# Optimization experiments

Measured on AMD Instinct MI355X. Metric: run time of the kernel, lower is better.

## Reference

```python
import jax, jax.numpy as jnp
import numpy as np

B, DIM, H, W = 8, 64, 128, 128
HEADS = 8
HID = DIM * 2          # ffn_expansion_factor = 2
DCONV = DIM // 4       # partial-conv channels
EPS_LN = 1e-5
EPS_NRM = 1e-12

def _conv(x, w, groups=1):
    # stride-1 conv, SAME padding (matches padding=1 for k=3, padding=0 for k=1)
    return jax.lax.conv_general_dilated(
        x, w, (1, 1), 'SAME',
        dimension_numbers=('NCHW', 'OIHW', 'NCHW'),
        feature_group_count=groups)

def _ln_channel(x, w, b):
    # WithBias LayerNorm over channel dim (to_3d puts c last, normalize last dim)
    mu = x.mean(axis=1, keepdims=True)
    var = ((x - mu) ** 2).mean(axis=1, keepdims=True)
    return (x - mu) / jnp.sqrt(var + EPS_LN) * w[None, :, None, None] + b[None, :, None, None]

def setup_inputs() -> dict:
    key = jax.random.key(0)
    ks = jax.random.split(key, 8)
    s = 0.02
    return {
        'x': jax.random.normal(ks[0], (B, DIM, H, W), jnp.float32),
        'ln1_w': jnp.ones((DIM,), jnp.float32),
        'ln1_b': jnp.zeros((DIM,), jnp.float32),
        'qkv_w': jax.random.normal(ks[1], (3 * DIM, DIM, 1, 1), jnp.float32) * s,
        'qkv_dw_w': jax.random.normal(ks[2], (3 * DIM, 1, 3, 3), jnp.float32) * s,
        'temperature': jnp.ones((HEADS, 1, 1), jnp.float32),
        'attn_mix': jnp.ones((2,), jnp.float32),
        'proj_w': jax.random.normal(ks[3], (DIM, DIM, 1, 1), jnp.float32) * s,
        'ln2_w': jnp.ones((DIM,), jnp.float32),
        'ln2_b': jnp.zeros((DIM,), jnp.float32),
        'pconv_w': jax.random.normal(ks[4], (DCONV, DCONV, 3, 3), jnp.float32) * s,
        'pin_w': jax.random.normal(ks[5], (2 * HID, DIM, 1, 1), jnp.float32) * s,
        'dw_w': jax.random.normal(ks[6], (HID, 1, 3, 3), jnp.float32) * s,
        'pout_w': jax.random.normal(ks[7], (DIM, HID, 1, 1), jnp.float32) * s,
    }

def reference(x, ln1_w, ln1_b, qkv_w, qkv_dw_w, temperature, attn_mix,
              proj_w, ln2_w, ln2_b, pconv_w, pin_w, dw_w, pout_w):
    b, c, h, w = x.shape
    ch = c // HEADS
    # ---- TwinPeakAttention on norm1(x) ----
    y = _ln_channel(x, ln1_w, ln1_b)
    qkv = _conv(_conv(y, qkv_w), qkv_dw_w, groups=3 * c)
    q, k, v = jnp.split(qkv, 3, axis=1)
    rs = lambda t: t.reshape(b, HEADS, ch, h * w)          # b head c (h w)
    q, k, v = rs(q), rs(k), rs(v)
    q = q / jnp.maximum(jnp.linalg.norm(q, axis=-1, keepdims=True), EPS_NRM)
    k = k / jnp.maximum(jnp.linalg.norm(k, axis=-1, keepdims=True), EPS_NRM)
    scores = jnp.einsum('bhcn,bhdn->bhcd', q, k)           # [b, head, ch, ch]
    attn_sm = jax.nn.softmax(scores * temperature[None], axis=-1)
    attn_relu = jnp.maximum(scores, 0.0) ** 2
    wmix = jax.nn.softmax(attn_mix)
    attn = wmix[0] * attn_sm + wmix[1] * attn_relu
    out = jnp.einsum('bhcd,bhdn->bhcn', attn, v).reshape(b, c, h, w)
    x = x + _conv(out, proj_w)
    # ---- FDFN on norm2(x) ----
    y = _ln_channel(x, ln2_w, ln2_b)
    y = jnp.concatenate([_conv(y[:, :DCONV], pconv_w), y[:, DCONV:]], axis=1)
    y = _conv(y, pin_w)                                    # [b, 2*HID, h, w]
    a, g = jnp.split(y, 2, axis=1)
    a = _conv(a, dw_w, groups=HID)
    y = _conv(jax.nn.gelu(a, approximate=False) * g, pout_w)
    return x + y
```

## Files before the change

kernel.cpp:

```cpp
#include <hip/hip_runtime.h>
#include <math.h>

#define NPIX 16384
#define B_ 8

typedef __attribute__((ext_vector_type(4))) float f32x4;
typedef __attribute__((ext_vector_type(8))) short bf16x8;
typedef __attribute__((ext_vector_type(4))) unsigned int u32x4;

__device__ inline unsigned short f2bf(float f) {
  unsigned int u = __builtin_bit_cast(unsigned int, f);
  return (unsigned short)((u + 0x7fffu + ((u >> 16) & 1u)) >> 16);
}
__device__ inline float bf2f(unsigned short h) {
  unsigned int u = ((unsigned int)h) << 16;
  return __builtin_bit_cast(float, u);
}
__device__ inline unsigned int pack2(unsigned short a, unsigned short b) {
  return (unsigned int)a | ((unsigned int)b << 16);
}
__device__ inline f32x4 mfma16(bf16x8 a, bf16x8 b, f32x4 c) {
  return __builtin_amdgcn_mfma_f32_16x16x32_bf16(a, b, c, 0, 0, 0);
}
__device__ inline void unpack8(u32x4 u, float* f) {
#pragma unroll
  for (int i = 0; i < 4; ++i) {
    unsigned int w = u[i];
    f[2 * i]     = __builtin_bit_cast(float, w << 16);
    f[2 * i + 1] = __builtin_bit_cast(float, w & 0xffff0000u);
  }
}


__global__ __launch_bounds__(256) void k0_prep(
    const float* __restrict__ wq, const float* __restrict__ lw,
    const float* __restrict__ lb, const float* __restrict__ pin,
    const float* __restrict__ pout, unsigned short* __restrict__ wq2,
    float* __restrict__ s1, float* __restrict__ s2,
    unsigned short* __restrict__ pinb, unsigned short* __restrict__ pob) {
  int bid = blockIdx.x, t = threadIdx.x;
  if (bid == 0) {
    if (t < 192) {
      int co = t;
      float a = 0.f, bsum = 0.f;
      for (int ci = 0; ci < 64; ++ci) {
        float w = wq[co * 64 + ci];
        unsigned short hb = f2bf(w * lw[ci]);
        wq2[co * 64 + ci] = hb;
        a += bf2f(hb);
        bsum = fmaf(w, lb[ci], bsum);
      }
      s1[co] = a;
      s2[co] = bsum;
    }
  } else if (bid <= 64) {
    int i = (bid - 1) * 256 + t;
    pinb[i] = f2bf(pin[i]);
  } else {
    int i = (bid - 65) * 256 + t;
    pob[i] = f2bf(pout[i]);
  }
}

__global__ __launch_bounds__(256) void k1_qkv(
    const float* __restrict__ x, const unsigned short* __restrict__ wq2,
    const float* __restrict__ s1, const float* __restrict__ s2,
    unsigned short* __restrict__ qkv) {
  __shared__ __align__(16) unsigned char lx[64 * 128];
  __shared__ float sumL[4][64], sqL[4][64], muL[64], rsL[64];
  __shared__ __align__(16) unsigned short epi[4][16][72];
  int t = threadIdx.x, blk = blockIdx.x;
  int b = blk >> 8, hw0 = (blk & 255) * 64;
  const float* xb = x + (size_t)b * 64 * NPIX + hw0;
  int p = t & 63, g8 = t >> 6;
  float psum = 0.f, psq = 0.f;
#pragma unroll
  for (int r = 0; r < 2; ++r) {
    int ci0 = g8 * 8 + r * 32;
    float v[8];
#pragma unroll
    for (int j = 0; j < 8; ++j) {
      v[j] = xb[(size_t)(ci0 + j) * NPIX + p];
      psum += v[j];
      psq = fmaf(v[j], v[j], psq);
    }
    u32x4 pk;
#pragma unroll
    for (int j = 0; j < 4; ++j) pk[j] = pack2(f2bf(v[2 * j]), f2bf(v[2 * j + 1]));
    unsigned int addr = ((unsigned)(p * 128 + ci0 * 2)) ^ ((p & 7) << 4);
    *(u32x4*)&lx[addr] = pk;
  }
  sumL[g8][p] = psum;
  sqL[g8][p] = psq;
  __syncthreads();
  if (t < 64) {
    float s = sumL[0][t] + sumL[1][t] + sumL[2][t] + sumL[3][t];
    float q = sqL[0][t] + sqL[1][t] + sqL[2][t] + sqL[3][t];
    float mu = s * (1.f / 64.f);
    float var = q * (1.f / 64.f) - mu * mu;
    muL[t] = mu;
    rsL[t] = rsqrtf(fmaxf(var, 0.f) + 1e-5f);
  }
  __syncthreads();
  int lane = t & 63, wv = t >> 6, l16 = lane & 15, g = lane >> 4;
  int co0 = wv * 48;
  bf16x8 A[3][2];
#pragma unroll
  for (int ct = 0; ct < 3; ++ct) {
    int co = co0 + ct * 16 + l16;
#pragma unroll
    for (int kh = 0; kh < 2; ++kh)
      A[ct][kh] = *(const bf16x8*)(wq2 + (size_t)co * 64 + kh * 32 + g * 8);
  }
  f32x4 acc[3][4];
#pragma unroll
  for (int ct = 0; ct < 3; ++ct)
#pragma unroll
    for (int nt = 0; nt < 4; ++nt) acc[ct][nt] = (f32x4)0.f;
#pragma unroll
  for (int nt = 0; nt < 4; ++nt) {
    int pp = nt * 16 + l16;
#pragma unroll
    for (int kh = 0; kh < 2; ++kh) {
      unsigned int addr = ((unsigned)(pp * 128 + (kh * 32 + g * 8) * 2)) ^ ((pp & 7) << 4);
      bf16x8 Bf = *(const bf16x8*)&lx[addr];
#pragma unroll
      for (int ct = 0; ct < 3; ++ct) acc[ct][nt] = mfma16(A[ct][kh], Bf, acc[ct][nt]);
    }
  }
  int row1 = hw0 >> 7, wb1 = hw0 & 127;
  unsigned short* ob = qkv + ((size_t)(b * 128 + row1) * 192) * 128 + wb1;
#pragma unroll
  for (int ct = 0; ct < 3; ++ct) {
#pragma unroll
    for (int r = 0; r < 4; ++r) {
      int co = co0 + ct * 16 + g * 4 + r;
      float s1v = s1[co], s2v = s2[co];
#pragma unroll
      for (int nt = 0; nt < 4; ++nt) {
        int pl = nt * 16 + l16;
        float val = (acc[ct][nt][r] - muL[pl] * s1v) * rsL[pl] + s2v;
        epi[wv][g * 4 + r][pl] = f2bf(val);
      }
    }
#pragma unroll
    for (int i = 0; i < 2; ++i) {
      int chunk = i * 64 + lane, co_l = chunk >> 3, oct = chunk & 7;
      u32x4 v = *(const u32x4*)&epi[wv][co_l][oct * 8];
      *(u32x4*)(ob + (size_t)(co0 + ct * 16 + co_l) * 128 + oct * 8) = v;
    }
  }
}

__global__ __launch_bounds__(256) void k2_dw3x3(
    const unsigned short* __restrict__ in, const float* __restrict__ w9,
    unsigned short* __restrict__ out) {
  int blk0 = blockIdx.x;
  int blk = (blk0 & 7) * 1536 + (blk0 >> 3);
  int id = blk * 256 + threadIdx.x;
  int oct = id & 15;
  int cr = id >> 4;
  int ch = cr % 192;
  int br = cr / 192;
  int row = br & 127;
  int w0 = oct * 8;
  const float* wp = w9 + ch * 9;
  float wgt[9];
#pragma unroll
  for (int j = 0; j < 9; ++j) wgt[j] = wp[j];
  float rowv[3][10];
#pragma unroll
  for (int dy = 0; dy < 3; ++dy) {
#pragma unroll
    for (int i = 0; i < 10; ++i) rowv[dy][i] = 0.f;
    int hh = row + dy - 1;
    if ((unsigned)hh < 128u) {
      const unsigned short* rp = in + ((size_t)(br + dy - 1) * 192 + ch) * 128 + w0;
      u32x4 m = *(const u32x4*)rp;
      unpack8(m, &rowv[dy][1]);
      if (w0 > 0) rowv[dy][0] = bf2f(rp[-1]);
      if (w0 < 120) rowv[dy][9] = bf2f(rp[8]);
    }
  }
  u32x4 res;
#pragma unroll
  for (int i = 0; i < 8; i += 2) {
    float a0 = 0.f, a1 = 0.f;
#pragma unroll
    for (int dy = 0; dy < 3; ++dy)
#pragma unroll
      for (int dx = 0; dx < 3; ++dx) {
        a0 = fmaf(wgt[dy * 3 + dx], rowv[dy][i + dx], a0);
        a1 = fmaf(wgt[dy * 3 + dx], rowv[dy][i + 1 + dx], a1);
      }
    res[i >> 1] = pack2(f2bf(a0), f2bf(a1));
  }
  *(u32x4*)(out + ((size_t)br * 192 + ch) * 128 + w0) = res;
}

__global__ __launch_bounds__(256) void k3a_mfma(
    const unsigned short* __restrict__ qkvd, float* __restrict__ parts) {
  __shared__ float red[4][640];
  int blk = blockIdx.x;
  int b = blk >> 6, chunk = blk & 63;
  int t = threadIdx.x;
  int lane = t & 63, wv = t >> 6, l16 = lane & 15, g = lane >> 4;
  const unsigned short* bb = qkvd + (size_t)(b * 128) * 192 * 128;
  int n0 = chunk * 256 + wv * 64;
  f32x4 S[4], QQ[4], KK[4];
#pragma unroll
  for (int i = 0; i < 4; ++i) { S[i] = (f32x4)0.f; QQ[i] = (f32x4)0.f; KK[i] = (f32x4)0.f; }
#pragma unroll
  for (int ks = 0; ks < 2; ++ks) {
    int k0 = n0 + ks * 32 + g * 8;
    int r = k0 >> 7, w = k0 & 127;
    const unsigned short* rowb = bb + ((size_t)r * 192) * 128 + w;
    bf16x8 Q[4], K[4];
#pragma unroll
    for (int t4 = 0; t4 < 4; ++t4) {
      Q[t4] = *(const bf16x8*)(rowb + (size_t)(t4 * 16 + l16) * 128);
      K[t4] = *(const bf16x8*)(rowb + (size_t)(64 + t4 * 16 + l16) * 128);
    }
#pragma unroll
    for (int t4 = 0; t4 < 4; ++t4) {
      S[t4]  = mfma16(Q[t4], K[t4], S[t4]);
      QQ[t4] = mfma16(Q[t4], Q[t4], QQ[t4]);
      KK[t4] = mfma16(K[t4], K[t4], KK[t4]);
    }
  }
  int hi = l16 >> 3;
#pragma unroll
  for (int t4 = 0; t4 < 4; ++t4) {
#pragma unroll
    for (int r = 0; r < 4; ++r) {
      int m = g * 4 + r;
      if ((m >> 3) == hi) {
        int head = 2 * t4 + hi;
        red[wv][head * 80 + 16 + (m & 7) * 8 + (l16 & 7)] = S[t4][r];
      }
      if (m == l16) {
        int c = t4 * 16 + l16;
        red[wv][(c >> 3) * 80 + (c & 7)] = QQ[t4][r];
        red[wv][(c >> 3) * 80 + 8 + (c & 7)] = KK[t4][r];
      }
    }
  }
  __syncthreads();
  float* pb = parts + (size_t)blk * 640;
  for (int i = t; i < 640; i += 256)
    pb[i] = red[0][i] + red[1][i] + red[2][i] + red[3][i];
}

__global__ __launch_bounds__(256) void k3bc(
    const float* __restrict__ parts, const float* __restrict__ temp,
    const float* __restrict__ mix, const float* __restrict__ pw,
    unsigned short* __restrict__ M) {
  int b = blockIdx.x, t = threadIdx.x;
  __shared__ float s[8][80];
  __shared__ float att[8][64];
  for (int i = t; i < 640; i += 256) {
    const float* pbase = parts + (size_t)b * 64 * 640 + i;
    float v = 0.f;
    for (int c = 0; c < 64; ++c) v += pbase[c * 640];
    s[i / 80][i % 80] = v;
  }
  __syncthreads();
  float m0 = fmaxf(mix[0], mix[1]);
  float e0 = expf(mix[0] - m0), e1 = expf(mix[1] - m0);
  float w0 = e0 / (e0 + e1), w1 = e1 / (e0 + e1);
  for (int i = t; i < 512; i += 256) {
    int head = i >> 6, e = i & 63, c = e >> 3, d = e & 7;
    float tt = temp[head];
    float rq = 1.f / fmaxf(sqrtf(s[head][c]), 1e-12f);
    float sc[8];
    float mx = -1e30f;
#pragma unroll
    for (int d2 = 0; d2 < 8; ++d2) {
      float rk = 1.f / fmaxf(sqrtf(s[head][8 + d2]), 1e-12f);
      sc[d2] = s[head][16 + c * 8 + d2] * rq * rk;
      mx = fmaxf(mx, sc[d2] * tt);
    }
    float sum = 0.f;
#pragma unroll
    for (int d2 = 0; d2 < 8; ++d2) sum += expf(sc[d2] * tt - mx);
    float sm = expf(sc[d] * tt - mx) / sum;
    float r = fmaxf(sc[d], 0.f);
    r = r * r;
    att[head][e] = w0 * sm + w1 * r;
  }
  __syncthreads();
  for (int i = t; i < 4096; i += 256) {
    int co = i >> 6, ci = i & 63, head = ci >> 3, d = ci & 7;
    float a = 0.f;
#pragma unroll
    for (int cc = 0; cc < 8; ++cc)
      a = fmaf(pw[co * 64 + head * 8 + cc], att[head][cc * 8 + d], a);
    M[(size_t)b * 4096 + i] = f2bf(a);
  }
}

__global__ __launch_bounds__(256) void k4_av(
    const unsigned short* __restrict__ qkvd, const unsigned short* __restrict__ Mb,
    const float* __restrict__ x, const float* __restrict__ lw,
    const float* __restrict__ lb, unsigned short* __restrict__ x1,
    unsigned short* __restrict__ y2) {
  __shared__ __align__(16) unsigned char lv[64 * 128];
  __shared__ float sumL[4][64], sqL[4][64], muL[64], rsL[64];
  int t = threadIdx.x, blk = blockIdx.x;
  int b = blk >> 8, hw0 = (blk & 255) * 64;
  int row4 = hw0 >> 7, wb4 = hw0 & 127;
  const unsigned short* vb = qkvd + ((size_t)(b * 128 + row4) * 192 + 128) * 128 + wb4;
  int p = t & 63, g8 = t >> 6;
#pragma unroll
  for (int r = 0; r < 2; ++r) {
    int ci0 = g8 * 8 + r * 32;
    unsigned short hh[8];
#pragma unroll
    for (int j = 0; j < 8; ++j) hh[j] = vb[(size_t)(ci0 + j) * 128 + p];
    u32x4 pk;
#pragma unroll
    for (int j = 0; j < 4; ++j) pk[j] = pack2(hh[2 * j], hh[2 * j + 1]);
    unsigned int addr = ((unsigned)(p * 128 + ci0 * 2)) ^ ((p & 7) << 4);
    *(u32x4*)&lv[addr] = pk;
  }
  __syncthreads();
  int lane = t & 63, wv = t >> 6, l16 = lane & 15, g = lane >> 4;
  bf16x8 A[2];
#pragma unroll
  for (int kh = 0; kh < 2; ++kh)
    A[kh] = *(const bf16x8*)(Mb + (size_t)b * 4096 + (size_t)(wv * 16 + l16) * 64 + kh * 32 + g * 8);
  f32x4 acc[4];
#pragma unroll
  for (int nt = 0; nt < 4; ++nt) acc[nt] = (f32x4)0.f;
#pragma unroll
  for (int nt = 0; nt < 4; ++nt) {
    int pp = nt * 16 + l16;
#pragma unroll
    for (int kh = 0; kh < 2; ++kh) {
      unsigned int addr = ((unsigned)(pp * 128 + (kh * 32 + g * 8) * 2)) ^ ((pp & 7) << 4);
      bf16x8 Bf = *(const bf16x8*)&lv[addr];
      acc[nt] = mfma16(A[kh], Bf, acc[nt]);
    }
  }
  const float* xb = x + (size_t)b * 64 * NPIX + hw0;
  unsigned short* x1b = x1 + (size_t)b * 64 * NPIX + hw0;
  float vals[4][4];
#pragma unroll
  for (int nt = 0; nt < 4; ++nt) {
    float ps = 0.f, pq = 0.f;
#pragma unroll
    for (int r = 0; r < 4; ++r) {
      int co = wv * 16 + g * 4 + r;
      size_t idx = (size_t)co * NPIX + nt * 16 + l16;
      float a = acc[nt][r] + xb[idx];
      vals[nt][r] = a;
      x1b[idx] = f2bf(a);
      ps += a;
      pq = fmaf(a, a, pq);
    }
    ps += __shfl_xor(ps, 16); ps += __shfl_xor(ps, 32);
    pq += __shfl_xor(pq, 16); pq += __shfl_xor(pq, 32);
    if (g == 0) { sumL[wv][nt * 16 + l16] = ps; sqL[wv][nt * 16 + l16] = pq; }
  }
  __syncthreads();
  if (t < 64) {
    float s = sumL[0][t] + sumL[1][t] + sumL[2][t] + sumL[3][t];
    float q = sqL[0][t] + sqL[1][t] + sqL[2][t] + sqL[3][t];
    float mu = s * (1.f / 64.f);
    float var = q * (1.f / 64.f) - mu * mu;
    muL[t] = mu;
    rsL[t] = rsqrtf(fmaxf(var, 0.f) + 1e-5f);
  }
  __syncthreads();
  unsigned short* y2b = y2 + (size_t)b * 64 * NPIX + hw0;
#pragma unroll
  for (int nt = 0; nt < 4; ++nt)
#pragma unroll
    for (int r = 0; r < 4; ++r) {
      int co = wv * 16 + g * 4 + r;
      int pl = nt * 16 + l16;
      float yv = (vals[nt][r] - muL[pl]) * rsL[pl] * lw[co] + lb[co];
      y2b[(size_t)co * NPIX + pl] = f2bf(yv);
    }
}

__global__ __launch_bounds__(256) void k5_pconv(
    const unsigned short* __restrict__ y2, const float* __restrict__ pcw,
    unsigned short* __restrict__ pc) {
  __shared__ unsigned short ly[16 * 120];
  int t = threadIdx.x, blk = blockIdx.x;
  int b = blk >> 8, tile = blk & 255;
  int ty = tile >> 4, tx = tile & 15;
  int h0 = ty * 8, w0 = tx * 8;
  const unsigned short* yb = y2 + (size_t)b * 64 * NPIX;
  for (int i = t; i < 1600; i += 256) {
    int ci = i / 100, r = i - ci * 100;
    int hy = r / 10, hx = r - hy * 10;
    int gh = h0 - 1 + hy, gw = w0 - 1 + hx;
    unsigned short v = 0;
    if ((unsigned)gh < 128u && (unsigned)gw < 128u) v = yb[(size_t)ci * NPIX + gh * 128 + gw];
    ly[ci * 120 + hy * 12 + hx] = v;
  }
  __syncthreads();
  int lp = t & 63;
  int py = lp >> 3, px = lp & 7;
  int cq = __builtin_amdgcn_readfirstlane(t >> 6);
  int co0 = cq * 4;
  float a0 = 0.f, a1 = 0.f, a2 = 0.f, a3 = 0.f;
  for (int ci = 0; ci < 16; ++ci) {
    float nb[9];
#pragma unroll
    for (int ky = 0; ky < 3; ++ky)
#pragma unroll
      for (int kx = 0; kx < 3; ++kx)
        nb[ky * 3 + kx] = bf2f(ly[ci * 120 + (py + ky) * 12 + px + kx]);
    const float* wp = pcw + (co0 * 16 + ci) * 9;
#pragma unroll
    for (int k = 0; k < 9; ++k) {
      a0 = fmaf(wp[k],       nb[k], a0);
      a1 = fmaf(wp[144 + k], nb[k], a1);
      a2 = fmaf(wp[288 + k], nb[k], a2);
      a3 = fmaf(wp[432 + k], nb[k], a3);
    }
  }
  size_t obase = (size_t)b * 16 * NPIX + (h0 + py) * 128 + w0 + px;
  pc[obase + (size_t)(co0 + 0) * NPIX] = f2bf(a0);
  pc[obase + (size_t)(co0 + 1) * NPIX] = f2bf(a1);
  pc[obase + (size_t)(co0 + 2) * NPIX] = f2bf(a2);
  pc[obase + (size_t)(co0 + 3) * NPIX] = f2bf(a3);
}

__global__ __launch_bounds__(256) void k6_pin(
    const unsigned short* __restrict__ pc, const unsigned short* __restrict__ y2,
    const unsigned short* __restrict__ pinb, unsigned short* __restrict__ ag) {
  __shared__ __align__(16) unsigned char bt[64 * 128];
  __shared__ __align__(16) unsigned short epi[4][16][72];
  int t = threadIdx.x, blk = blockIdx.x;
  int b = blk >> 8, hw0 = (blk & 255) * 64;
  int px = t & 63, cb = t >> 6;
  {
    const unsigned short* base = (cb == 0) ? (pc + (size_t)b * 16 * NPIX)
                                           : (y2 + (size_t)b * 64 * NPIX);
#pragma unroll
    for (int j = 0; j < 16; j += 2) {
      int ch = cb * 16 + j;
      unsigned short v0 = base[(size_t)ch * NPIX + hw0 + px];
      unsigned short v1 = base[(size_t)(ch + 1) * NPIX + hw0 + px];
      unsigned int addr = ((unsigned)(px * 128 + ch * 2)) ^ ((px & 7) << 4);
      *(unsigned int*)&bt[addr] = pack2(v0, v1);
    }
  }
  __syncthreads();
  int lane = t & 63, wv = t >> 6, l16 = lane & 15, g = lane >> 4;
  bf16x8 A[4][2];
#pragma unroll
  for (int ct = 0; ct < 4; ++ct) {
    int co = wv * 64 + ct * 16 + l16;
#pragma unroll
    for (int kh = 0; kh < 2; ++kh)
      A[ct][kh] = *(const bf16x8*)(pinb + (size_t)co * 64 + kh * 32 + g * 8);
  }
  f32x4 acc[4][4];
#pragma unroll
  for (int ct = 0; ct < 4; ++ct)
#pragma unroll
    for (int nt = 0; nt < 4; ++nt) acc[ct][nt] = (f32x4)0.f;
#pragma unroll
  for (int nt = 0; nt < 4; ++nt) {
    int pp = nt * 16 + l16;
#pragma unroll
    for (int kh = 0; kh < 2; ++kh) {
      unsigned int addr = ((unsigned)(pp * 128 + (kh * 32 + g * 8) * 2)) ^ ((pp & 7) << 4);
      bf16x8 Bf = *(const bf16x8*)&bt[addr];
#pragma unroll
      for (int ct = 0; ct < 4; ++ct) acc[ct][nt] = mfma16(A[ct][kh], Bf, acc[ct][nt]);
    }
  }
  int row6 = hw0 >> 7, wb6 = hw0 & 127;
  unsigned short* ab = ag + ((size_t)(b * 128 + row6) * 256) * 128 + wb6;
#pragma unroll
  for (int ct = 0; ct < 4; ++ct) {
#pragma unroll
    for (int nt = 0; nt < 4; ++nt)
#pragma unroll
      for (int r = 0; r < 4; ++r)
        epi[wv][g * 4 + r][nt * 16 + l16] = f2bf(acc[ct][nt][r]);
#pragma unroll
    for (int i = 0; i < 2; ++i) {
      int chunk = i * 64 + lane, co_l = chunk >> 3, oct = chunk & 7;
      u32x4 v = *(const u32x4*)&epi[wv][co_l][oct * 8];
      int co = wv * 64 + ct * 16 + co_l;
      *(u32x4*)(ab + (size_t)co * 128 + oct * 8) = v;
    }
  }
}

__global__ __launch_bounds__(256) void k7_fdfn(
    const unsigned short* __restrict__ ag, const float* __restrict__ dww,
    const unsigned short* __restrict__ pob, const unsigned short* __restrict__ x1,
    float* __restrict__ out) {
  __shared__ __align__(16) unsigned char bt[64 * 256];
  __shared__ float dwl[1152];
  int t = threadIdx.x;
  int blk0 = blockIdx.x;
  int blk = (blk0 & 7) * 256 + (blk0 >> 3);
  int b = blk >> 8, rr = blk & 255;
  int row = rr >> 1, w0t = (rr & 1) * 64;
  for (int i = t; i < 1152; i += 256) dwl[i] = dww[i];
  __syncthreads();
#pragma unroll 1
  for (int it = 0; it < 2; ++it) {
    int idx = it * 256 + t;
    int chp = idx >> 3, oct = idx & 7;
    int ch0 = chp * 2;
    int w0 = w0t + oct * 8;
    float rowa[2][3][10];
    float gt[2][8];
#pragma unroll
    for (int cc = 0; cc < 2; ++cc) {
      int ch = ch0 + cc;
#pragma unroll
      for (int dy = 0; dy < 3; ++dy) {
#pragma unroll
        for (int i2 = 0; i2 < 10; ++i2) rowa[cc][dy][i2] = 0.f;
        int hh = row + dy - 1;
        if ((unsigned)hh < 128u) {
          const unsigned short* rp = ag + ((size_t)(b * 128 + hh) * 256 + ch) * 128 + w0;
          unpack8(*(const u32x4*)rp, &rowa[cc][dy][1]);
          if (w0 > 0) rowa[cc][dy][0] = bf2f(rp[-1]);
          if (w0 < 120) rowa[cc][dy][9] = bf2f(rp[8]);
        }
      }
      unpack8(*(const u32x4*)(ag + ((size_t)(b * 128 + row) * 256 + 128 + ch) * 128 + w0), gt[cc]);
    }
    float wgt[2][9];
#pragma unroll
    for (int cc = 0; cc < 2; ++cc)
#pragma unroll
      for (int j = 0; j < 9; ++j) wgt[cc][j] = dwl[(ch0 + cc) * 9 + j];
#pragma unroll
    for (int i2 = 0; i2 < 8; ++i2) {
      unsigned short h2[2];
#pragma unroll
      for (int cc = 0; cc < 2; ++cc) {
        float a = 0.f;
#pragma unroll
        for (int dy = 0; dy < 3; ++dy)
#pragma unroll
          for (int dx = 0; dx < 3; ++dx)
            a = fmaf(wgt[cc][dy * 3 + dx], rowa[cc][dy][i2 + dx], a);
        float gl = 0.5f * a * (1.f + erff(a * 0.70710678118654752f)) * gt[cc][i2];
        h2[cc] = f2bf(gl);
      }
      int pxl = oct * 8 + i2;
      unsigned int f = (unsigned)(((pxl & 7) ^ (pxl >> 3)) << 4);
      unsigned int addr = (unsigned)(pxl * 256) + (((unsigned)(ch0 * 2)) ^ f);
      *(unsigned int*)&bt[addr] = pack2(h2[0], h2[1]);
    }
  }
  __syncthreads();
  int lane = t & 63, wv = t >> 6, l16 = lane & 15, g = lane >> 4;
  bf16x8 A[4];
#pragma unroll
  for (int kh = 0; kh < 4; ++kh)
    A[kh] = *(const bf16x8*)(pob + (size_t)(wv * 16 + l16) * 128 + kh * 32 + g * 8);
  f32x4 acc[4];
#pragma unroll
  for (int nt = 0; nt < 4; ++nt) acc[nt] = (f32x4)0.f;
#pragma unroll
  for (int nt = 0; nt < 4; ++nt) {
    int pp = nt * 16 + l16;
    unsigned int f = (unsigned)(((pp & 7) ^ (pp >> 3)) << 4);
#pragma unroll
    for (int kh = 0; kh < 4; ++kh) {
      unsigned int addr = (unsigned)(pp * 256) + (((unsigned)((kh * 32 + g * 8) * 2)) ^ f);
      bf16x8 Bf = *(const bf16x8*)&bt[addr];
      acc[nt] = mfma16(A[kh], Bf, acc[nt]);
    }
  }
  __syncthreads();
  float* ebuf = (float*)&bt[wv * 4096];
#pragma unroll
  for (int nt = 0; nt < 4; ++nt)
#pragma unroll
    for (int r = 0; r < 4; ++r)
      ebuf[(g * 4 + r) * 64 + nt * 16 + l16] = acc[nt][r];
  const unsigned short* x1b = x1 + (size_t)b * 64 * NPIX + row * 128 + w0t;
  float* ob = out + (size_t)b * 64 * NPIX + row * 128 + w0t;
#pragma unroll
  for (int i = 0; i < 4; ++i) {
    int chunk = i * 64 + lane;
    int co_l = chunk >> 4, q4 = (chunk & 15) * 4;
    f32x4 v = *(const f32x4*)&ebuf[co_l * 64 + q4];
    int co = wv * 16 + co_l;
    uint2 xv = *(const uint2*)(x1b + (size_t)co * NPIX + q4);
    f32x4 o;
    o[0] = v[0] + bf2f((unsigned short)(xv.x & 0xffffu));
    o[1] = v[1] + bf2f((unsigned short)(xv.x >> 16));
    o[2] = v[2] + bf2f((unsigned short)(xv.y & 0xffffu));
    o[3] = v[3] + bf2f((unsigned short)(xv.y >> 16));
    *(f32x4*)(ob + (size_t)co * NPIX + q4) = o;
  }
}

extern "C" void kernel_launch(void* const* d_in, const int* in_sizes, int n_in,
                              void* d_out, int out_size, void* d_ws, size_t ws_size,
                              hipStream_t stream) {
  const float* x       = (const float*)d_in[0];
  const float* ln1_w   = (const float*)d_in[1];
  const float* ln1_b   = (const float*)d_in[2];
  const float* qkv_w   = (const float*)d_in[3];
  const float* qkv_dww = (const float*)d_in[4];
  const float* temp    = (const float*)d_in[5];
  const float* mix     = (const float*)d_in[6];
  const float* proj_w  = (const float*)d_in[7];
  const float* ln2_w   = (const float*)d_in[8];
  const float* ln2_b   = (const float*)d_in[9];
  const float* pconv_w = (const float*)d_in[10];
  const float* pin_w   = (const float*)d_in[11];
  const float* dw_w    = (const float*)d_in[12];
  const float* pout_w  = (const float*)d_in[13];
  float* out = (float*)d_out;

  if (ws_size < (size_t)117515776) return;
  char* w8 = (char*)d_ws;
  unsigned short* qkv  = (unsigned short*)(w8 + 0);
  unsigned short* qkvd = (unsigned short*)(w8 + 50331648);
  unsigned short* x1   = (unsigned short*)(w8 + 100663296);
  unsigned short* wq2  = (unsigned short*)(w8 + 117440512);
  float*          s1   = (float*)(w8 + 117465088);
  float*          s2   = (float*)(w8 + 117465856);
  unsigned short* pinb = (unsigned short*)(w8 + 117466624);
  unsigned short* pob  = (unsigned short*)(w8 + 117499392);
  float*          parts= (float*)(w8 + 0);
  unsigned short* M    = (unsigned short*)(w8 + 2097152);
  unsigned short* y2   = (unsigned short*)(w8 + 4194304);
  unsigned short* pc   = (unsigned short*)(w8 + 20971520);
  unsigned short* ag   = (unsigned short*)(w8 + 33554432);

  k0_prep<<<97, 256, 0, stream>>>(qkv_w, ln1_w, ln1_b, pin_w, pout_w, wq2, s1, s2, pinb, pob);
  k1_qkv<<<2048, 256, 0, stream>>>(x, wq2, s1, s2, qkv);
  k2_dw3x3<<<12288, 256, 0, stream>>>(qkv, qkv_dww, qkvd);
  k3a_mfma<<<512, 256, 0, stream>>>(qkvd, parts);
  k3bc<<<8, 256, 0, stream>>>(parts, temp, mix, proj_w, M);
  k4_av<<<2048, 256, 0, stream>>>(qkvd, M, x, ln2_w, ln2_b, x1, y2);
  k5_pconv<<<2048, 256, 0, stream>>>(y2, pconv_w, pc);
  k6_pin<<<2048, 256, 0, stream>>>(pc, y2, pinb, ag);
  k7_fdfn<<<2048, 256, 0, stream>>>(ag, dw_w, pob, x1, out);
}
```

Measured before the change: 175.2 us.

## Halve k7 pixel tile and issue all global loads before weight sync

```diff
diff --git a/kernel.cpp b/kernel.cpp
--- a/kernel.cpp
+++ b/kernel.cpp
@@ -499,63 +499,71 @@
     const unsigned short* __restrict__ ag, const float* __restrict__ dww,
     const unsigned short* __restrict__ pob, const unsigned short* __restrict__ x1,
     float* __restrict__ out) {
-  __shared__ __align__(16) unsigned char bt[64 * 256];
+  __shared__ __align__(16) unsigned char bt[32 * 256];
   __shared__ float dwl[1152];
   int t = threadIdx.x;
   int blk0 = blockIdx.x;
-  int blk = (blk0 & 7) * 256 + (blk0 >> 3);
-  int b = blk >> 8, rr = blk & 255;
-  int row = rr >> 1, w0t = (rr & 1) * 64;
+  int blk = (blk0 & 7) * 512 + (blk0 >> 3);
+  int b = blk >> 9, rr = blk & 511;
+  int row = rr >> 2, w0t = (rr & 3) * 32;
   for (int i = t; i < 1152; i += 256) dwl[i] = dww[i];
-  __syncthreads();
-#pragma unroll 1
-  for (int it = 0; it < 2; ++it) {
-    int idx = it * 256 + t;
-    int chp = idx >> 3, oct = idx & 7;
-    int ch0 = chp * 2;
-    int w0 = w0t + oct * 8;
-    float rowa[2][3][10];
-    float gt[2][8];
+
+  int chp = t >> 2, oct = t & 3;
+  int ch0 = chp * 2;
+  int w0 = w0t + oct * 8;
+  bool hasL = (w0 > 0), hasR = (w0 < 120);
+  u32x4 arow[2][3];
+  u32x4 grow[2];
+  unsigned short eL[2][3], eR[2][3];
+#pragma unroll
+  for (int cc = 0; cc < 2; ++cc) {
+    int ch = ch0 + cc;
+    grow[cc] = *(const u32x4*)(ag + ((size_t)(b * 128 + row) * 256 + 128 + ch) * 128 + w0);
+#pragma unroll
+    for (int dy = 0; dy < 3; ++dy) {
+      int hh = row + dy - 1;
+      bool v = (unsigned)hh < 128u;
+      const unsigned short* rp = ag + ((size_t)(b * 128 + hh) * 256 + ch) * 128 + w0;
+      arow[cc][dy] = v ? *(const u32x4*)rp : (u32x4)0u;
+      eL[cc][dy] = (v && hasL) ? rp[-1] : (unsigned short)0;
+      eR[cc][dy] = (v && hasR) ? rp[8] : (unsigned short)0;
+    }
+  }
+  __syncthreads();
+
+  {
+    unsigned short hv[2][8];
 #pragma unroll
     for (int cc = 0; cc < 2; ++cc) {
-      int ch = ch0 + cc;
+      float rowa[3][10], gt[8];
 #pragma unroll
       for (int dy = 0; dy < 3; ++dy) {
-#pragma unroll
-        for (int i2 = 0; i2 < 10; ++i2) rowa[cc][dy][i2] = 0.f;
-        int hh = row + dy - 1;
-        if ((unsigned)hh < 128u) {
-          const unsigned short* rp = ag + ((size_t)(b * 128 + hh) * 256 + ch) * 128 + w0;
-          unpack8(*(const u32x4*)rp, &rowa[cc][dy][1]);
-          if (w0 > 0) rowa[cc][dy][0] = bf2f(rp[-1]);
-          if (w0 < 120) rowa[cc][dy][9] = bf2f(rp[8]);
-        }
+        rowa[dy][0] = bf2f(eL[cc][dy]);
+        unpack8(arow[cc][dy], &rowa[dy][1]);
+        rowa[dy][9] = bf2f(eR[cc][dy]);
       }
-      unpack8(*(const u32x4*)(ag + ((size_t)(b * 128 + row) * 256 + 128 + ch) * 128 + w0), gt[cc]);
-    }
-    float wgt[2][9];
-#pragma unroll
-    for (int cc = 0; cc < 2; ++cc)
-#pragma unroll
-      for (int j = 0; j < 9; ++j) wgt[cc][j] = dwl[(ch0 + cc) * 9 + j];
+      unpack8(grow[cc], gt);
+      float wgt[9];
+#pragma unroll
+      for (int j = 0; j < 9; ++j) wgt[j] = dwl[(ch0 + cc) * 9 + j];
+#pragma unroll
+      for (int i2 = 0; i2 < 8; ++i2) {
+        float a = 0.f;
+#pragma unroll
+        for (int dy = 0; dy < 3; ++dy)
+#pragma unroll
+          for (int dx = 0; dx < 3; ++dx)
+            a = fmaf(wgt[dy * 3 + dx], rowa[dy][i2 + dx], a);
+        float gl = 0.5f * a * (1.f + erff(a * 0.70710678118654752f)) * gt[i2];
+        hv[cc][i2] = f2bf(gl);
+      }
+    }
 #pragma unroll
     for (int i2 = 0; i2 < 8; ++i2) {
-      unsigned short h2[2];
-#pragma unroll
-      for (int cc = 0; cc < 2; ++cc) {
-        float a = 0.f;
-#pragma unroll
-        for (int dy = 0; dy < 3; ++dy)
-#pragma unroll
-          for (int dx = 0; dx < 3; ++dx)
-            a = fmaf(wgt[cc][dy * 3 + dx], rowa[cc][dy][i2 + dx], a);
-        float gl = 0.5f * a * (1.f + erff(a * 0.70710678118654752f)) * gt[cc][i2];
-        h2[cc] = f2bf(gl);
-      }
       int pxl = oct * 8 + i2;
       unsigned int f = (unsigned)(((pxl & 7) ^ (pxl >> 3)) << 4);
       unsigned int addr = (unsigned)(pxl * 256) + (((unsigned)(ch0 * 2)) ^ f);
-      *(unsigned int*)&bt[addr] = pack2(h2[0], h2[1]);
+      *(unsigned int*)&bt[addr] = pack2(hv[0][i2], hv[1][i2]);
     }
   }
   __syncthreads();
@@ -564,11 +572,11 @@
 #pragma unroll
   for (int kh = 0; kh < 4; ++kh)
     A[kh] = *(const bf16x8*)(pob + (size_t)(wv * 16 + l16) * 128 + kh * 32 + g * 8);
-  f32x4 acc[4];
-#pragma unroll
-  for (int nt = 0; nt < 4; ++nt) acc[nt] = (f32x4)0.f;
-#pragma unroll
-  for (int nt = 0; nt < 4; ++nt) {
+  f32x4 acc[2];
+#pragma unroll
+  for (int nt = 0; nt < 2; ++nt) acc[nt] = (f32x4)0.f;
+#pragma unroll
+  for (int nt = 0; nt < 2; ++nt) {
     int pp = nt * 16 + l16;
     unsigned int f = (unsigned)(((pp & 7) ^ (pp >> 3)) << 4);
 #pragma unroll
@@ -579,19 +587,19 @@
     }
   }
   __syncthreads();
-  float* ebuf = (float*)&bt[wv * 4096];
-#pragma unroll
-  for (int nt = 0; nt < 4; ++nt)
+  float* ebuf = (float*)&bt[wv * 2048];
+#pragma unroll
+  for (int nt = 0; nt < 2; ++nt)
 #pragma unroll
     for (int r = 0; r < 4; ++r)
-      ebuf[(g * 4 + r) * 64 + nt * 16 + l16] = acc[nt][r];
+      ebuf[(g * 4 + r) * 32 + nt * 16 + l16] = acc[nt][r];
   const unsigned short* x1b = x1 + (size_t)b * 64 * NPIX + row * 128 + w0t;
   float* ob = out + (size_t)b * 64 * NPIX + row * 128 + w0t;
 #pragma unroll
-  for (int i = 0; i < 4; ++i) {
+  for (int i = 0; i < 2; ++i) {
     int chunk = i * 64 + lane;
-    int co_l = chunk >> 4, q4 = (chunk & 15) * 4;
-    f32x4 v = *(const f32x4*)&ebuf[co_l * 64 + q4];
+    int co_l = chunk >> 3, q4 = (chunk & 7) * 4;
+    f32x4 v = *(const f32x4*)&ebuf[co_l * 32 + q4];
     int co = wv * 16 + co_l;
     uint2 xv = *(const uint2*)(x1b + (size_t)co * NPIX + q4);
     f32x4 o;
@@ -646,5 +654,5 @@
   k4_av<<<2048, 256, 0, stream>>>(qkvd, M, x, ln2_w, ln2_b, x1, y2);
   k5_pconv<<<2048, 256, 0, stream>>>(y2, pconv_w, pc);
   k6_pin<<<2048, 256, 0, stream>>>(pc, y2, pinb, ag);
-  k7_fdfn<<<2048, 256, 0, stream>>>(ag, dw_w, pob, x1, out);
-}
+  k7_fdfn<<<4096, 256, 0, stream>>>(ag, dw_w, pob, x1, out);
+}
```

New measurement: 184.9 us. 1.06x slower.
